# Kernel tuning notes

Measured on AMD Instinct MI355X. Metric: run time of the kernel, lower is better.

Reference implementation:

```python
import jax, jax.numpy as jnp
import numpy as np

T = 25
H1, H2, H3 = 16, 72, 32


def _lin_params(key, out_dim, in_dim):
    k1, k2 = jax.random.split(key)
    s = 1.0 / np.sqrt(in_dim)
    W = jax.random.uniform(k1, (out_dim, in_dim), jnp.float32, -s, s)
    b = jax.random.uniform(k2, (out_dim,), jnp.float32, -s, s)
    return W, b


def _lstm_params(key, in_dim, hid):
    k1, k2, k3, k4 = jax.random.split(key, 4)
    s = 1.0 / np.sqrt(hid)
    Wih = jax.random.uniform(k1, (4 * hid, in_dim), jnp.float32, -s, s)
    Whh = jax.random.uniform(k2, (4 * hid, hid), jnp.float32, -s, s)
    bih = jax.random.uniform(k3, (4 * hid,), jnp.float32, -s, s)
    bhh = jax.random.uniform(k4, (4 * hid,), jnp.float32, -s, s)
    return Wih, Whh, bih, bhh


def setup_inputs() -> dict:
    key = jax.random.key(0)
    ks = jax.random.split(key, 9)
    B = 131072
    x = jax.random.normal(ks[0], (B, T, 2), jnp.float32)
    y = jax.random.normal(ks[1], (B, T, 36), jnp.float32)
    Wih1, Whh1, bih1, bhh1 = _lstm_params(ks[2], 2, H1)
    Wih2, Whh2, bih2, bhh2 = _lstm_params(ks[3], H2, H2)
    Wih3, Whh3, bih3, bhh3 = _lstm_params(ks[4], H1 + H2, H3)
    W1, b1 = _lin_params(ks[5], 64, 36)
    W2, b2 = _lin_params(ks[6], H2, 64)
    W3, b3 = _lin_params(ks[7], 16, H3)
    W4, b4 = _lin_params(ks[8], 2, 16)
    return dict(x=x, y=y,
                Wih1=Wih1, Whh1=Whh1, bih1=bih1, bhh1=bhh1,
                Wih2=Wih2, Whh2=Whh2, bih2=bih2, bhh2=bhh2,
                Wih3=Wih3, Whh3=Whh3, bih3=bih3, bhh3=bhh3,
                W1=W1, b1=b1, W2=W2, b2=b2, W3=W3, b3=b3, W4=W4, b4=b4)


def _lstm_cell(xt, h, c, Wih, Whh, bih, bhh):
    # PyTorch LSTMCell gate order: i, f, g, o
    g = xt @ Wih.T + bih + h @ Whh.T + bhh
    i, f, gg, o = jnp.split(g, 4, axis=-1)
    c_new = jax.nn.sigmoid(f) * c + jax.nn.sigmoid(i) * jnp.tanh(gg)
    h_new = jax.nn.sigmoid(o) * jnp.tanh(c_new)
    return h_new, c_new


def _forward(x, y, Wih1, Whh1, bih1, bhh1, Wih2, Whh2, bih2, bhh2,
             Wih3, Whh3, bih3, bhh3, W1, b1, W2, b2, W3, b3, W4, b4):
    B = x.shape[0]
    init = (jnp.zeros((B, H1), jnp.float32), jnp.zeros((B, H1), jnp.float32),
            jnp.zeros((B, H2), jnp.float32), jnp.zeros((B, H2), jnp.float32),
            jnp.zeros((B, H3), jnp.float32), jnp.zeros((B, H3), jnp.float32))

    def step(carry, inp):
        h1, c1, h2, c2, h3, c3 = carry
        xt, yt = inp  # [B,2], [B,36]
        h1, c1 = _lstm_cell(xt, h1, c1, Wih1, Whh1, bih1, bhh1)
        l2 = jax.nn.relu(yt @ W1.T + b1) @ W2.T + b2
        h2, c2 = _lstm_cell(l2, h2, c2, Wih2, Whh2, bih2, bhh2)
        h = jnp.concatenate([h1, h2], axis=1)
        h3, c3 = _lstm_cell(h, h3, c3, Wih3, Whh3, bih3, bhh3)
        out = jax.nn.relu(h3 @ W3.T + b3) @ W4.T + b4  # [B,2]
        return (h1, c1, h2, c2, h3, c3), out

    xs = (jnp.swapaxes(x, 0, 1), jnp.swapaxes(y, 0, 1))  # [T,B,*]
    _, outs = jax.lax.scan(step, init, xs)  # [T,B,2]
    # torch.cat(outputs, dim=1) -> [B, T*2]
    return jnp.swapaxes(outs, 0, 1).reshape(B, T * 2)


def reference(x, y, Wih1, Whh1, bih1, bhh1, Wih2, Whh2, bih2, bhh2,
              Wih3, Whh3, bih3, bhh3, W1, b1, W2, b2, W3, b3, W4, b4):
    return _forward(x, y, Wih1, Whh1, bih1, bhh1, Wih2, Whh2, bih2, bhh2,
                    Wih3, Whh3, bih3, bhh3, W1, b1, W2, b2, W3, b3, W4, b4)
```

## Files before the change

kernel.cpp:

```cpp
#include <hip/hip_runtime.h>
#include <hip/hip_bf16.h>

#define THREADS 768

typedef __hip_bfloat16 bf16;
typedef __attribute__((ext_vector_type(4))) float f32x4;
typedef __attribute__((ext_vector_type(8))) short bf16x8;

#define MFMA __builtin_amdgcn_mfma_f32_16x16x32_bf16

#define O_A1  0
#define O_AY  4096
#define O_AT1 12288
#define O_A2  20480
#define O_AH3 40960
#define LDS_ELEMS 45056
#define LDS_BYTES (LDS_ELEMS * 2)

__device__ __forceinline__ int kmap(int l, int j) {
    return (((l >> 4) & 3) << 2) + (j & 3) + ((j >> 2) << 4);
}
__device__ __forceinline__ int frag_off(int m, int k) {
    int l = (m & 15) | (((k >> 2) & 3) << 4);
    int j = (k & 3) | (((k >> 4) & 1) << 2);
    return (l << 3) + j;
}
__device__ __forceinline__ void st_frag(bf16* sbase, int KC, int m, int k, float v) {
    sbase[(((m >> 4) * KC + (k >> 5)) << 9) + frag_off(m, k & 31)] = __float2bfloat16(v);
}
__device__ __forceinline__ void st_frag_c(bf16* sbase, int KC, int m, int cidx, int kl, float v) {
    sbase[(((m >> 4) * KC + cidx) << 9) + frag_off(m, kl)] = __float2bfloat16(v);
}

__device__ __forceinline__ float rcp_(float x) { return __builtin_amdgcn_rcpf(x); }

__device__ __forceinline__ float lstm_ew1(f32x4 acc, float& cst) {
    float ei = __expf(-acc[0]);
    float ef = __expf(-acc[1]);
    float eg = __expf(2.0f * fminf(acc[2], 40.0f));
    float eo = __expf(-acc[3]);
    float c = rcp_(1.0f + ef) * cst + (eg - 1.0f) * rcp_((1.0f + ei) * (eg + 1.0f));
    cst = c;
    float ec = __expf(2.0f * fminf(c, 40.0f));
    return (ec - 1.0f) * rcp_((1.0f + eo) * (ec + 1.0f));
}

__device__ __forceinline__ ushort bfu(float f) {
    union { bf16 b; ushort u; } v; v.b = __float2bfloat16(f); return v.u;
}

template <typename F>
__device__ __forceinline__ bf16x8 mk_frag(int lane, F val) {
    union { bf16x8 v; bf16 h[8]; } u;
#pragma unroll
    for (int j = 0; j < 8; ++j) u.h[j] = __float2bfloat16(val(kmap(lane, j)));
    return u.v;
}

__global__ void __launch_bounds__(THREADS, 3)
lstm_fused(const float* __restrict__ x, const float* __restrict__ y,
           const float* __restrict__ Wih1, const float* __restrict__ Whh1,
           const float* __restrict__ bih1, const float* __restrict__ bhh1,
           const float* __restrict__ Wih2, const float* __restrict__ Whh2,
           const float* __restrict__ bih2, const float* __restrict__ bhh2,
           const float* __restrict__ Wih3, const float* __restrict__ Whh3,
           const float* __restrict__ bih3, const float* __restrict__ bhh3,
           const float* __restrict__ W1, const float* __restrict__ b1,
           const float* __restrict__ W2, const float* __restrict__ b2,
           const float* __restrict__ W3, const float* __restrict__ b3,
           const float* __restrict__ W4, const float* __restrict__ b4,
           float* __restrict__ out) {
    extern __shared__ char smem[];
    bf16* sb = (bf16*)smem;
    const int tid = threadIdx.x;
    const int wave = tid >> 6, lane = tid & 63, ln15 = lane & 15;
    const int b0 = blockIdx.x * 64;

    const bool HEAVY = wave < 6;
    const int ntL2a = HEAVY ? 2 * wave : 6 + wave;

    bf16x8 bL2[2][5];
    bf16x8 bL1 = {};
    bf16x8 bF1[2] = {};
    bf16x8 bF2[2] = {};
    bf16x8 bL3[5] = {};
    bf16x8 bF3 = {};

    {
        auto fillL2 = [&](int nt, bf16x8* dst) {
            int R = (nt << 4) + ln15;
            int r = (R & 3) * 72 + (R >> 2);
            float bias = bih2[r] + bhh2[r];
#pragma unroll
            for (int kc = 0; kc < 5; ++kc)
                dst[kc] = mk_frag(lane, [&](int kl) {
                    int k = kc * 32 + kl;
                    return k < 72 ? Wih2[r * 72 + k]
                         : (k < 144 ? Whh2[r * 72 + (k - 72)]
                         : (k == 144 ? bias : 0.0f)); });
        };
        fillL2(ntL2a, bL2[0]);
        if (HEAVY) fillL2(2 * wave + 1, bL2[1]);
        else { bL2[1][0] = bL2[0][0]; bL2[1][1] = bL2[0][0]; bL2[1][2] = bL2[0][0];
               bL2[1][3] = bL2[0][0]; bL2[1][4] = bL2[0][0]; }
    }
    if (wave >= 6 && wave < 10) {
        int R = ((wave - 6) << 4) + ln15;
        int r = (R & 3) * 16 + (R >> 2);
        float bias = bih1[r] + bhh1[r];
        bL1 = mk_frag(lane, [&](int k) {
            return k < 2 ? Wih1[r * 2 + k]
                 : (k < 18 ? Whh1[r * 16 + (k - 2)]
                 : (k == 18 ? bias : 0.0f)); });
    }
    if (wave >= 8) {
        int n = ((wave - 8) << 4) + ln15;
        float bias = b1[n];
#pragma unroll
        for (int kc = 0; kc < 2; ++kc)
            bF1[kc] = mk_frag(lane, [&](int kl) {
                int k = kc * 32 + kl;
                return k < 36 ? W1[n * 36 + k] : (k == 36 ? bias : 0.0f); });
    }
    if (wave >= 4) {
        int R = ((wave - 4) << 4) + ln15;
        int r = (R & 3) * 32 + (R >> 2);
        float bias = bih3[r] + bhh3[r];
        bL3[0] = mk_frag(lane, [&](int k) {
            return (k >= 2 && k < 18) ? Wih3[r * 88 + (k - 2)] : (k == 18 ? bias : 0.0f); });
        bL3[1] = mk_frag(lane, [&](int k) {
            return (k >= 8) ? Wih3[r * 88 + 8 + k] : 0.0f; });
        bL3[2] = mk_frag(lane, [&](int k) { return Wih3[r * 88 + 40 + k]; });
        bL3[3] = mk_frag(lane, [&](int k) {
            return (k < 16) ? Wih3[r * 88 + 72 + k] : 0.0f; });
        bL3[4] = mk_frag(lane, [&](int k) { return Whh3[r * 32 + k]; });
    }
    if (wave < 4 || wave == 7) {
        int nt2 = (wave == 7) ? 4 : wave;
        int n = (nt2 << 4) + ln15;
#pragma unroll
        for (int kc = 0; kc < 2; ++kc)
            bF2[kc] = mk_frag(lane, [&](int kl) {
                return (n < 72) ? W2[n * 64 + kc * 32 + kl] : 0.0f; });
    }
    if (wave < 4) bF3 = mk_frag(lane, [&](int k) { return W3[ln15 * 32 + k]; });

    {
        int4* z = (int4*)sb;
        int4 zv = {0, 0, 0, 0};
        for (int i = tid; i < LDS_BYTES / 16; i += THREADS) z[i] = zv;
    }
    __syncthreads();
    for (int it = tid; it < 2 * 2304; it += THREADS) {
        int slot = it / 2304, r2 = it - slot * 2304;
        int m = r2 / 36, k = r2 - m * 36;
        st_frag(sb + O_AY + ((slot * 8) << 9), 2, m, k,
                y[(size_t)(b0 + m) * 900 + slot * 36 + k]);
    }
    if (tid < 128) {
        int m = tid >> 1, k = tid & 1;
        st_frag(sb + O_A1, 1, m, k, x[(size_t)(b0 + m) * 50 + k]);
    }
    {
        const bf16 one = __float2bfloat16(1.0f);
        if (tid < 128) {
            int s = tid >> 6, mt = (tid >> 4) & 3, n = tid & 15;
            sb[O_A1 + ((s * 4 + mt) << 9) + frag_off(n, 18)] = one;
        } else if (tid < 256) {
            int i = tid - 128; int s = i >> 6, mt = (i >> 4) & 3, n = i & 15;
            sb[O_AY + ((s * 8 + mt * 2 + 1) << 9) + frag_off(n, 4)] = one;
        } else if (tid < 384) {
            int i = tid - 256; int s = i >> 6, mt = (i >> 4) & 3, n = i & 15;
            sb[O_A2 + ((mt * 10 + 8 + s) << 9) + frag_off(n, 16)] = one;
        }
    }
    __syncthreads();
    if (wave >= 8) {
        const int nf0 = ((wave - 8) << 4) + ((lane >> 4) << 2);
#pragma unroll
        for (int s = 0; s < 2; ++s) {
#pragma unroll
            for (int mt = 0; mt < 4; ++mt) {
                f32x4 acc = {0.f, 0.f, 0.f, 0.f};
#pragma unroll
                for (int kc = 0; kc < 2; ++kc) {
                    bf16x8 a = *(const bf16x8*)(sb + O_AY + ((s * 8 + mt * 2 + kc) << 9) + (lane << 3));
                    acc = MFMA(bF1[kc], a, acc, 0, 0, 0);
                }
                int batch = (mt << 4) + ln15;
#pragma unroll
                for (int r = 0; r < 4; ++r)
                    st_frag(sb + O_AT1 + (((s ^ 1) * 8) << 9), 2, batch, nf0 + r, fmaxf(acc[r], 0.0f));
            }
        }
    }
    __syncthreads();
    if (wave < 4 || wave == 7) {
        const int nt2 = (wave == 7) ? 4 : wave;
        const int nb = (nt2 << 4) + ((lane >> 4) << 2);
        float4 bv = {0.f, 0.f, 0.f, 0.f};
        if (nb < 72) bv = *(const float4*)(b2 + nb);
#pragma unroll
        for (int mt = 0; mt < 4; ++mt) {
            f32x4 acc = {0.f, 0.f, 0.f, 0.f};
#pragma unroll
            for (int kc = 0; kc < 2; ++kc) {
                bf16x8 a = *(const bf16x8*)(sb + O_AT1 + ((8 + mt * 2 + kc) << 9) + (lane << 3));
                acc = MFMA(bF2[kc], a, acc, 0, 0, 0);
            }
            if (nb < 72) {
                int batch = (mt << 4) + ln15;
#pragma unroll
                for (int r = 0; r < 4; ++r) {
                    int n = nb + r;
                    st_frag_c(sb + O_A2, 10, batch, ((n >> 5) << 1), n & 31, acc[r] + bv[r]);
                }
            }
        }
    } else if (wave >= 10) {
        const int m = ((wave - 10) << 5) + (lane >> 1);
        const int mt = m >> 4;
        const float* yp = y + (size_t)(b0 + m) * 900 + 2 * 36;
#pragma unroll
        for (int c = (lane & 1); c < 9; c += 2) {
            float4 v = *(const float4*)(yp + 4 * c);
            ushort4 pk;
            pk.x = bfu(v.x); pk.y = bfu(v.y); pk.z = bfu(v.z); pk.w = bfu(v.w);
            int k0 = 4 * c, kc = k0 >> 5;
            int l2v = (m & 15) | (((k0 >> 2) & 3) << 4);
            int j0 = ((k0 >> 4) & 1) << 2;
            *(ushort4*)((ushort*)(sb + O_AY) + ((mt * 2 + kc) << 9) + (l2v << 3) + j0) = pk;
        }
    }
    float c1[4] = {};
    float cs2[2][4] = {};
    float c3[4] = {};
    __syncthreads();

    for (int t = 0; t <= 25; ++t) {
        const int p = t & 1, q = p ^ 1;

        if (t <= 24) {
#pragma unroll
            for (int mt = 0; mt < 4; ++mt) {
                bf16x8 al[5];
#pragma unroll
                for (int b = 0; b < 5; ++b)
                    al[b] = *(const bf16x8*)(sb + O_A2 + ((mt * 10 + 2 * b + p) << 9) + (lane << 3));
                {
                    f32x4 acc = {0.f, 0.f, 0.f, 0.f};
#pragma unroll
                    for (int b = 0; b < 5; ++b) acc = MFMA(bL2[0][b], al[b], acc, 0, 0, 0);
                    float hv = lstm_ew1(acc, cs2[0][mt]);
                    int batch = (mt << 4) + ln15;
                    int k = 72 + (ntL2a << 2) + (lane >> 4);
                    st_frag_c(sb + O_A2, 10, batch, ((k >> 5) << 1) + q, k & 31, hv);
                }
                if (HEAVY) {
                    f32x4 acc = {0.f, 0.f, 0.f, 0.f};
#pragma unroll
                    for (int b = 0; b < 5; ++b) acc = MFMA(bL2[1][b], al[b], acc, 0, 0, 0);
                    float hv = lstm_ew1(acc, cs2[1][mt]);
                    int batch = (mt << 4) + ln15;
                    int k = 72 + ((2 * wave + 1) << 2) + (lane >> 4);
                    st_frag_c(sb + O_A2, 10, batch, ((k >> 5) << 1) + q, k & 31, hv);
                }
            }
        }

        if (t <= 24 && wave >= 6 && wave < 10) {
            const int nt1 = wave - 6;
#pragma unroll
            for (int mt = 0; mt < 4; ++mt) {
                bf16x8 a = *(const bf16x8*)(sb + O_A1 + ((p * 4 + mt) << 9) + (lane << 3));
                f32x4 acc = {0.f, 0.f, 0.f, 0.f};
                acc = MFMA(bL1, a, acc, 0, 0, 0);
                float hv = lstm_ew1(acc, c1[mt]);
                int batch = (mt << 4) + ln15;
                st_frag(sb + O_A1 + ((q * 4) << 9), 1, batch, 2 + (nt1 << 2) + (lane >> 4), hv);
            }
        }
        if (wave == 6 && t <= 23) {
            const int m = lane, mt = m >> 4;
            float2 xv = *(const float2*)(x + (size_t)(b0 + m) * 50 + (t + 1) * 2);
            union { uint u; ushort s[2]; } xu;
            xu.s[0] = bfu(xv.x); xu.s[1] = bfu(xv.y);
            *(uint*)((ushort*)(sb + O_A1) + ((q * 4 + mt) << 9) + ((m & 15) << 3)) = xu.u;
        }
        if (t <= 22 && wave >= 8) {
            const int nf0 = ((wave - 8) << 4) + ((lane >> 4) << 2);
#pragma unroll
            for (int mt = 0; mt < 4; ++mt) {
                f32x4 acc = {0.f, 0.f, 0.f, 0.f};
#pragma unroll
                for (int kc = 0; kc < 2; ++kc) {
                    bf16x8 a = *(const bf16x8*)(sb + O_AY + ((p * 8 + mt * 2 + kc) << 9) + (lane << 3));
                    acc = MFMA(bF1[kc], a, acc, 0, 0, 0);
                }
                int batch = (mt << 4) + ln15;
#pragma unroll
                for (int r = 0; r < 4; ++r)
                    st_frag(sb + O_AT1 + ((q * 8) << 9), 2, batch, nf0 + r, fmaxf(acc[r], 0.0f));
            }
        }
        if (wave >= 10 && t <= 21) {
            const int m = ((wave - 10) << 5) + (lane >> 1);
            const int mt = m >> 4;
            const float* yp = y + (size_t)(b0 + m) * 900 + (t + 3) * 36;
#pragma unroll
            for (int c = (lane & 1); c < 9; c += 2) {
                float4 v = *(const float4*)(yp + 4 * c);
                ushort4 pk;
                pk.x = bfu(v.x); pk.y = bfu(v.y); pk.z = bfu(v.z); pk.w = bfu(v.w);
                int k0 = 4 * c, kc = k0 >> 5;
                int l2v = (m & 15) | (((k0 >> 2) & 3) << 4);
                int j0 = ((k0 >> 4) & 1) << 2;
                *(ushort4*)((ushort*)(sb + O_AY) + ((q * 8 + mt * 2 + kc) << 9) + (l2v << 3) + j0) = pk;
            }
        }
        if (t >= 1 && wave >= 4) {
            const int nt3 = wave - 4;
#pragma unroll
            for (int mt = 0; mt < 4; ++mt) {
                f32x4 acc = {0.f, 0.f, 0.f, 0.f};
                bf16x8 a0 = *(const bf16x8*)(sb + O_A1 + ((p * 4 + mt) << 9) + (lane << 3));
                acc = MFMA(bL3[0], a0, acc, 0, 0, 0);
#pragma unroll
                for (int j = 0; j < 3; ++j) {
                    bf16x8 a = *(const bf16x8*)(sb + O_A2 + ((mt * 10 + 4 + 2 * j + p) << 9) + (lane << 3));
                    acc = MFMA(bL3[1 + j], a, acc, 0, 0, 0);
                }
                bf16x8 a4 = *(const bf16x8*)(sb + O_AH3 + ((p * 4 + mt) << 9) + (lane << 3));
                acc = MFMA(bL3[4], a4, acc, 0, 0, 0);
                float hv = lstm_ew1(acc, c3[mt]);
                int batch = (mt << 4) + ln15;
                st_frag(sb + O_AH3 + ((q * 4) << 9), 1, batch, (nt3 << 2) + (lane >> 4), hv);
            }
        }
        if (t <= 23 && (wave < 4 || wave == 7)) {
            const int nt2 = (wave == 7) ? 4 : wave;
            const int nb = (nt2 << 4) + ((lane >> 4) << 2);
            float4 bv = {0.f, 0.f, 0.f, 0.f};
            if (nb < 72) bv = *(const float4*)(b2 + nb);
#pragma unroll
            for (int mt = 0; mt < 4; ++mt) {
                f32x4 acc = {0.f, 0.f, 0.f, 0.f};
#pragma unroll
                for (int kc = 0; kc < 2; ++kc) {
                    bf16x8 a = *(const bf16x8*)(sb + O_AT1 + ((p * 8 + mt * 2 + kc) << 9) + (lane << 3));
                    acc = MFMA(bF2[kc], a, acc, 0, 0, 0);
                }
                if (nb < 72) {
                    int batch = (mt << 4) + ln15;
#pragma unroll
                    for (int r = 0; r < 4; ++r) {
                        int n = nb + r;
                        st_frag_c(sb + O_A2, 10, batch, ((n >> 5) << 1) + q, n & 31, acc[r] + bv[r]);
                    }
                }
            }
        }
        if (t >= 2 && wave < 4) {
            const int mt = wave, qd = lane >> 4;
            float4 b3v = *(const float4*)(b3 + 4 * qd);
            float4 w0v = *(const float4*)(W4 + 4 * qd);
            float4 w1v = *(const float4*)(W4 + 16 + 4 * qd);
            bf16x8 bb = *(const bf16x8*)(sb + O_AH3 + ((p * 4 + mt) << 9) + (lane << 3));
            f32x4 acc = {0.f, 0.f, 0.f, 0.f};
            acc = MFMA(bF3, bb, acc, 0, 0, 0);
            float s0 = 0.f, s1 = 0.f;
#pragma unroll
            for (int r = 0; r < 4; ++r) {
                float u = fmaxf(acc[r] + b3v[r], 0.0f);
                s0 = fmaf(u, w0v[r], s0);
                s1 = fmaf(u, w1v[r], s1);
            }
            s0 += __shfl_xor(s0, 16); s0 += __shfl_xor(s0, 32);
            s1 += __shfl_xor(s1, 16); s1 += __shfl_xor(s1, 32);
            if (lane < 16) {
                float2 o; o.x = s0 + b4[0]; o.y = s1 + b4[1];
                *(float2*)(out + (size_t)(b0 + (mt << 4) + lane) * 50 + (t - 2) * 2) = o;
            }
        }
        __syncthreads();
    }

    if (wave < 4) {
        const int mt = wave, qd = lane >> 4;
        float4 b3v = *(const float4*)(b3 + 4 * qd);
        float4 w0v = *(const float4*)(W4 + 4 * qd);
        float4 w1v = *(const float4*)(W4 + 16 + 4 * qd);
        bf16x8 bb = *(const bf16x8*)(sb + O_AH3 + (mt << 9) + (lane << 3));
        f32x4 acc = {0.f, 0.f, 0.f, 0.f};
        acc = MFMA(bF3, bb, acc, 0, 0, 0);
        float s0 = 0.f, s1 = 0.f;
#pragma unroll
        for (int r = 0; r < 4; ++r) {
            float u = fmaxf(acc[r] + b3v[r], 0.0f);
            s0 = fmaf(u, w0v[r], s0);
            s1 = fmaf(u, w1v[r], s1);
        }
        s0 += __shfl_xor(s0, 16); s0 += __shfl_xor(s0, 32);
        s1 += __shfl_xor(s1, 16); s1 += __shfl_xor(s1, 32);
        if (lane < 16) {
            float2 o; o.x = s0 + b4[0]; o.y = s1 + b4[1];
            *(float2*)(out + (size_t)(b0 + (mt << 4) + lane) * 50 + 24 * 2) = o;
        }
    }
}

extern "C" void kernel_launch(void* const* d_in, const int* in_sizes, int n_in,
                              void* d_out, int out_size, void* d_ws, size_t ws_size,
                              hipStream_t stream) {
    (void)in_sizes; (void)n_in; (void)d_ws; (void)ws_size; (void)out_size;
    hipFuncSetAttribute((const void*)lstm_fused,
                        hipFuncAttributeMaxDynamicSharedMemorySize, LDS_BYTES);
    lstm_fused<<<dim3(2048), dim3(THREADS), LDS_BYTES, stream>>>(
        (const float*)d_in[0], (const float*)d_in[1],
        (const float*)d_in[2], (const float*)d_in[3],
        (const float*)d_in[4], (const float*)d_in[5],
        (const float*)d_in[6], (const float*)d_in[7],
        (const float*)d_in[8], (const float*)d_in[9],
        (const float*)d_in[10], (const float*)d_in[11],
        (const float*)d_in[12], (const float*)d_in[13],
        (const float*)d_in[14], (const float*)d_in[15],
        (const float*)d_in[16], (const float*)d_in[17],
        (const float*)d_in[18], (const float*)d_in[19],
        (const float*)d_in[20], (const float*)d_in[21],
        (float*)d_out);
}
```

Measured before the change: 1.001 ms.

## Switch to 32x32x16 MFMA with 16-wave role partitioning per block

Replaces the 16x16x32 bf16 MFMA tiles with 32x32x16 tiles, which changes the LDS fragment layout to a 32-column block scheme. The block grows from 12 to 16 waves, and the work is reassigned: waves 0-8 run LSTM2, waves 9-12 run LSTM3, the output head and the y prefetch, and waves 13-15 run LSTM1, the first linear layer and the second linear layer. Launch bounds go to 4 blocks of 1024 threads. The goal is fewer MFMA instructions and better balance across waves in the recurrent loop, at the cost of higher register pressure and a tighter occupancy target.

```diff
diff --git a/kernel.cpp b/kernel.cpp
--- a/kernel.cpp
+++ b/kernel.cpp
@@ -1,35 +1,29 @@
 #include <hip/hip_runtime.h>
 #include <hip/hip_bf16.h>
 
-#define THREADS 768
+#define THREADS 1024
 
 typedef __hip_bfloat16 bf16;
 typedef __attribute__((ext_vector_type(4))) float f32x4;
+typedef __attribute__((ext_vector_type(16))) float f32x16;
 typedef __attribute__((ext_vector_type(8))) short bf16x8;
 
-#define MFMA __builtin_amdgcn_mfma_f32_16x16x32_bf16
+#define MFMA32 __builtin_amdgcn_mfma_f32_32x32x16_bf16
+#define Z16 f32x16{0.f,0.f,0.f,0.f,0.f,0.f,0.f,0.f,0.f,0.f,0.f,0.f,0.f,0.f,0.f,0.f}
 
 #define O_A1  0
 #define O_AY  4096
-#define O_AT1 12288
+#define O_AT1 10240
 #define O_A2  20480
 #define O_AH3 40960
 #define LDS_ELEMS 45056
 #define LDS_BYTES (LDS_ELEMS * 2)
 
-__device__ __forceinline__ int kmap(int l, int j) {
-    return (((l >> 4) & 3) << 2) + (j & 3) + ((j >> 2) << 4);
-}
-__device__ __forceinline__ int frag_off(int m, int k) {
-    int l = (m & 15) | (((k >> 2) & 3) << 4);
-    int j = (k & 3) | (((k >> 4) & 1) << 2);
-    return (l << 3) + j;
-}
-__device__ __forceinline__ void st_frag(bf16* sbase, int KC, int m, int k, float v) {
-    sbase[(((m >> 4) * KC + (k >> 5)) << 9) + frag_off(m, k & 31)] = __float2bfloat16(v);
-}
-__device__ __forceinline__ void st_frag_c(bf16* sbase, int KC, int m, int cidx, int kl, float v) {
-    sbase[(((m >> 4) * KC + cidx) << 9) + frag_off(m, kl)] = __float2bfloat16(v);
+__device__ __forceinline__ int blk(int KC, int nt, int kc, int slot) {
+    return ((nt * KC + kc) * 2 + slot) << 9;
+}
+__device__ __forceinline__ int eix(int col, int kl) {
+    return ((col | ((kl >> 3) << 5)) << 3) + (kl & 7);
 }
 
 __device__ __forceinline__ float rcp_(float x) { return __builtin_amdgcn_rcpf(x); }
@@ -50,14 +44,15 @@
 }
 
 template <typename F>
-__device__ __forceinline__ bf16x8 mk_frag(int lane, F val) {
+__device__ __forceinline__ bf16x8 mk32(int lane, F val) {
     union { bf16x8 v; bf16 h[8]; } u;
 #pragma unroll
-    for (int j = 0; j < 8; ++j) u.h[j] = __float2bfloat16(val(kmap(lane, j)));
+    for (int j = 0; j < 8; ++j)
+        u.h[j] = __float2bfloat16(val(((lane >> 5) << 3) + j));
     return u.v;
 }
 
-__global__ void __launch_bounds__(THREADS, 3)
+__global__ void __launch_bounds__(THREADS, 4)
 lstm_fused(const float* __restrict__ x, const float* __restrict__ y,
            const float* __restrict__ Wih1, const float* __restrict__ Whh1,
            const float* __restrict__ bih1, const float* __restrict__ bhh1,
@@ -73,77 +68,77 @@
     extern __shared__ char smem[];
     bf16* sb = (bf16*)smem;
     const int tid = threadIdx.x;
-    const int wave = tid >> 6, lane = tid & 63, ln15 = lane & 15;
+    const int wave = tid >> 6, lane = tid & 63;
+    const int ln31 = lane & 31, hi = lane >> 5;
     const int b0 = blockIdx.x * 64;
 
-    const bool HEAVY = wave < 6;
-    const int ntL2a = HEAVY ? 2 * wave : 6 + wave;
-
-    bf16x8 bL2[2][5];
-    bf16x8 bL1 = {};
-    bf16x8 bF1[2] = {};
-    bf16x8 bF2[2] = {};
-    bf16x8 bL3[5] = {};
-    bf16x8 bF3 = {};
-
-    {
-        auto fillL2 = [&](int nt, bf16x8* dst) {
-            int R = (nt << 4) + ln15;
-            int r = (R & 3) * 72 + (R >> 2);
-            float bias = bih2[r] + bhh2[r];
+    bf16x8 W[11];
+#pragma unroll
+    for (int i = 0; i < 11; ++i) W[i] = bf16x8{0, 0, 0, 0, 0, 0, 0, 0};
+
+    if (wave < 9) {
+        int n = 32 * wave + ln31;
+        int r = (n & 3) * 72 + (n >> 2);
+        float bias = bih2[r] + bhh2[r];
+#pragma unroll
+        for (int kc = 0; kc < 10; ++kc)
+            W[kc] = mk32(lane, [&](int k) {
+                int kg = kc * 16 + k;
+                return kg < 72 ? Wih2[r * 72 + kg]
+                     : (kg < 144 ? Whh2[r * 72 + (kg - 72)]
+                     : (kg == 144 ? bias : 0.0f)); });
+    } else if (wave < 13) {
+        int n = 32 * (wave - 9) + ln31;
+        int r = (n & 3) * 32 + (n >> 2);
+        float bias = bih3[r] + bhh3[r];
+        W[0] = mk32(lane, [&](int k) {
+            return k < 2 ? 0.0f : Wih3[r * 88 + (k - 2)]; });
+        W[1] = mk32(lane, [&](int k) {
+            int kg = 16 + k;
+            return kg < 18 ? Wih3[r * 88 + (kg - 2)] : (kg == 18 ? bias : 0.0f); });
+#pragma unroll
+        for (int i = 0; i < 5; ++i)
+            W[2 + i] = mk32(lane, [&](int k) {
+                int kg = 64 + i * 16 + k;
+                return kg < 72 ? 0.0f : Wih3[r * 88 + 16 + (kg - 72)]; });
+#pragma unroll
+        for (int i = 0; i < 2; ++i)
+            W[7 + i] = mk32(lane, [&](int k) { return Whh3[r * 32 + i * 16 + k]; });
+        if (wave < 11) {
+#pragma unroll
+            for (int i = 0; i < 2; ++i)
+                W[9 + i] = mk32(lane, [&](int k) {
+                    return (ln31 < 16) ? W3[ln31 * 32 + i * 16 + k] : 0.0f; });
+        }
+    } else {
+        if (wave < 15) {
+            int n = 32 * (wave - 13) + ln31;
+            int r = (n & 3) * 16 + (n >> 2);
+            float bias = bih1[r] + bhh1[r];
+            W[0] = mk32(lane, [&](int k) {
+                return k < 2 ? Wih1[r * 2 + k] : Whh1[r * 16 + (k - 2)]; });
+            W[1] = mk32(lane, [&](int k) {
+                int kg = 16 + k;
+                return kg < 18 ? Whh1[r * 16 + (kg - 2)] : (kg == 18 ? bias : 0.0f); });
+        }
+        {
+            int n2 = 32 * (wave - 13) + ln31;
 #pragma unroll
             for (int kc = 0; kc < 5; ++kc)
-                dst[kc] = mk_frag(lane, [&](int kl) {
-                    int k = kc * 32 + kl;
-                    return k < 72 ? Wih2[r * 72 + k]
-                         : (k < 144 ? Whh2[r * 72 + (k - 72)]
-                         : (k == 144 ? bias : 0.0f)); });
-        };
-        fillL2(ntL2a, bL2[0]);
-        if (HEAVY) fillL2(2 * wave + 1, bL2[1]);
-        else { bL2[1][0] = bL2[0][0]; bL2[1][1] = bL2[0][0]; bL2[1][2] = bL2[0][0];
-               bL2[1][3] = bL2[0][0]; bL2[1][4] = bL2[0][0]; }
-    }
-    if (wave >= 6 && wave < 10) {
-        int R = ((wave - 6) << 4) + ln15;
-        int r = (R & 3) * 16 + (R >> 2);
-        float bias = bih1[r] + bhh1[r];
-        bL1 = mk_frag(lane, [&](int k) {
-            return k < 2 ? Wih1[r * 2 + k]
-                 : (k < 18 ? Whh1[r * 16 + (k - 2)]
-                 : (k == 18 ? bias : 0.0f)); });
-    }
-    if (wave >= 8) {
-        int n = ((wave - 8) << 4) + ln15;
-        float bias = b1[n];
-#pragma unroll
-        for (int kc = 0; kc < 2; ++kc)
-            bF1[kc] = mk_frag(lane, [&](int kl) {
-                int k = kc * 32 + kl;
-                return k < 36 ? W1[n * 36 + k] : (k == 36 ? bias : 0.0f); });
-    }
-    if (wave >= 4) {
-        int R = ((wave - 4) << 4) + ln15;
-        int r = (R & 3) * 32 + (R >> 2);
-        float bias = bih3[r] + bhh3[r];
-        bL3[0] = mk_frag(lane, [&](int k) {
-            return (k >= 2 && k < 18) ? Wih3[r * 88 + (k - 2)] : (k == 18 ? bias : 0.0f); });
-        bL3[1] = mk_frag(lane, [&](int k) {
-            return (k >= 8) ? Wih3[r * 88 + 8 + k] : 0.0f; });
-        bL3[2] = mk_frag(lane, [&](int k) { return Wih3[r * 88 + 40 + k]; });
-        bL3[3] = mk_frag(lane, [&](int k) {
-            return (k < 16) ? Wih3[r * 88 + 72 + k] : 0.0f; });
-        bL3[4] = mk_frag(lane, [&](int k) { return Whh3[r * 32 + k]; });
-    }
-    if (wave < 4 || wave == 7) {
-        int nt2 = (wave == 7) ? 4 : wave;
-        int n = (nt2 << 4) + ln15;
-#pragma unroll
-        for (int kc = 0; kc < 2; ++kc)
-            bF2[kc] = mk_frag(lane, [&](int kl) {
-                return (n < 72) ? W2[n * 64 + kc * 32 + kl] : 0.0f; });
-    }
-    if (wave < 4) bF3 = mk_frag(lane, [&](int k) { return W3[ln15 * 32 + k]; });
+                W[2 + kc] = mk32(lane, [&](int k) {
+                    int kg = kc * 16 + k;
+                    if (n2 >= 72) return 0.0f;
+                    return kg < 64 ? W2[n2 * 64 + kg] : (kg == 64 ? b2[n2] : 0.0f); });
+        }
+        if (wave >= 14) {
+            int f = 32 * (wave - 14) + ln31;
+#pragma unroll
+            for (int kc = 0; kc < 3; ++kc)
+                W[7 + kc] = mk32(lane, [&](int k) {
+                    int kg = kc * 16 + k;
+                    return kg < 36 ? W1[f * 36 + kg] : (kg == 36 ? b1[f] : 0.0f); });
+        }
+    }
 
     {
         int4* z = (int4*)sb;
@@ -154,257 +149,278 @@
     for (int it = tid; it < 2 * 2304; it += THREADS) {
         int slot = it / 2304, r2 = it - slot * 2304;
         int m = r2 / 36, k = r2 - m * 36;
-        st_frag(sb + O_AY + ((slot * 8) << 9), 2, m, k,
-                y[(size_t)(b0 + m) * 900 + slot * 36 + k]);
+        sb[O_AY + blk(3, m >> 5, k >> 4, slot) + eix(m & 31, k & 15)] =
+            __float2bfloat16(y[(size_t)(b0 + m) * 900 + slot * 36 + k]);
     }
     if (tid < 128) {
         int m = tid >> 1, k = tid & 1;
-        st_frag(sb + O_A1, 1, m, k, x[(size_t)(b0 + m) * 50 + k]);
+        sb[O_A1 + blk(2, m >> 5, 0, 0) + eix(m & 31, k)] =
+            __float2bfloat16(x[(size_t)(b0 + m) * 50 + k]);
     }
     {
         const bf16 one = __float2bfloat16(1.0f);
-        if (tid < 128) {
-            int s = tid >> 6, mt = (tid >> 4) & 3, n = tid & 15;
-            sb[O_A1 + ((s * 4 + mt) << 9) + frag_off(n, 18)] = one;
-        } else if (tid < 256) {
-            int i = tid - 128; int s = i >> 6, mt = (i >> 4) & 3, n = i & 15;
-            sb[O_AY + ((s * 8 + mt * 2 + 1) << 9) + frag_off(n, 4)] = one;
-        } else if (tid < 384) {
-            int i = tid - 256; int s = i >> 6, mt = (i >> 4) & 3, n = i & 15;
-            sb[O_A2 + ((mt * 10 + 8 + s) << 9) + frag_off(n, 16)] = one;
-        }
+        int i = tid & 127, col = i & 31, nt = (i >> 5) & 1, s = (i >> 6) & 1;
+        if (tid < 128)       sb[O_A1 + blk(2, nt, 1, s) + eix(col, 2)] = one;
+        else if (tid < 256)  sb[O_AY + blk(3, nt, 2, s) + eix(col, 4)] = one;
+        else if (tid < 384)  sb[O_AT1 + blk(5, nt, 4, s) + eix(col, 0)] = one;
+        else if (tid < 512)  sb[O_A2 + blk(10, nt, 9, s) + eix(col, 0)] = one;
     }
     __syncthreads();
-    if (wave >= 8) {
-        const int nf0 = ((wave - 8) << 4) + ((lane >> 4) << 2);
+    if (wave >= 14) {
 #pragma unroll
         for (int s = 0; s < 2; ++s) {
 #pragma unroll
-            for (int mt = 0; mt < 4; ++mt) {
-                f32x4 acc = {0.f, 0.f, 0.f, 0.f};
-#pragma unroll
-                for (int kc = 0; kc < 2; ++kc) {
-                    bf16x8 a = *(const bf16x8*)(sb + O_AY + ((s * 8 + mt * 2 + kc) << 9) + (lane << 3));
-                    acc = MFMA(bF1[kc], a, acc, 0, 0, 0);
-                }
-                int batch = (mt << 4) + ln15;
-#pragma unroll
-                for (int r = 0; r < 4; ++r)
-                    st_frag(sb + O_AT1 + (((s ^ 1) * 8) << 9), 2, batch, nf0 + r, fmaxf(acc[r], 0.0f));
+            for (int nt = 0; nt < 2; ++nt) {
+                f32x16 acc = Z16;
+#pragma unroll
+                for (int kc = 0; kc < 3; ++kc) {
+                    bf16x8 a = *(const bf16x8*)(sb + O_AY + blk(3, nt, kc, s) + (lane << 3));
+                    acc = MFMA32(W[7 + kc], a, acc, 0, 0, 0);
+                }
+#pragma unroll
+                for (int qq = 0; qq < 4; ++qq) {
+                    int f0 = 32 * (wave - 14) + 8 * qq + 4 * hi;
+                    ushort4 pk;
+                    pk.x = bfu(fmaxf(acc[4 * qq + 0], 0.f));
+                    pk.y = bfu(fmaxf(acc[4 * qq + 1], 0.f));
+                    pk.z = bfu(fmaxf(acc[4 * qq + 2], 0.f));
+                    pk.w = bfu(fmaxf(acc[4 * qq + 3], 0.f));
+                    *(ushort4*)(sb + O_AT1 + blk(5, nt, f0 >> 4, s ^ 1) + eix(ln31, f0 & 15)) = pk;
+                }
             }
         }
     }
     __syncthreads();
-    if (wave < 4 || wave == 7) {
-        const int nt2 = (wave == 7) ? 4 : wave;
-        const int nb = (nt2 << 4) + ((lane >> 4) << 2);
-        float4 bv = {0.f, 0.f, 0.f, 0.f};
-        if (nb < 72) bv = *(const float4*)(b2 + nb);
-#pragma unroll
-        for (int mt = 0; mt < 4; ++mt) {
-            f32x4 acc = {0.f, 0.f, 0.f, 0.f};
-#pragma unroll
-            for (int kc = 0; kc < 2; ++kc) {
-                bf16x8 a = *(const bf16x8*)(sb + O_AT1 + ((8 + mt * 2 + kc) << 9) + (lane << 3));
-                acc = MFMA(bF2[kc], a, acc, 0, 0, 0);
-            }
-            if (nb < 72) {
-                int batch = (mt << 4) + ln15;
-#pragma unroll
-                for (int r = 0; r < 4; ++r) {
-                    int n = nb + r;
-                    st_frag_c(sb + O_A2, 10, batch, ((n >> 5) << 1), n & 31, acc[r] + bv[r]);
-                }
-            }
-        }
-    } else if (wave >= 10) {
-        const int m = ((wave - 10) << 5) + (lane >> 1);
-        const int mt = m >> 4;
+    if (wave >= 13) {
+#pragma unroll
+        for (int nt = 0; nt < 2; ++nt) {
+            f32x16 acc = Z16;
+#pragma unroll
+            for (int kc = 0; kc < 5; ++kc) {
+                bf16x8 a = *(const bf16x8*)(sb + O_AT1 + blk(5, nt, kc, 1) + (lane << 3));
+                acc = MFMA32(W[2 + kc], a, acc, 0, 0, 0);
+            }
+#pragma unroll
+            for (int qq = 0; qq < 4; ++qq) {
+                int n0 = 32 * (wave - 13) + 8 * qq + 4 * hi;
+                if (n0 < 72) {
+                    ushort4 pk;
+                    pk.x = bfu(acc[4 * qq + 0]); pk.y = bfu(acc[4 * qq + 1]);
+                    pk.z = bfu(acc[4 * qq + 2]); pk.w = bfu(acc[4 * qq + 3]);
+                    *(ushort4*)(sb + O_A2 + blk(10, nt, n0 >> 4, 0) + eix(ln31, n0 & 15)) = pk;
+                }
+            }
+        }
+    } else if (wave == 11 || wave == 12) {
+        const int half = wave - 11;
+        const int m = 32 * half + (lane >> 1);
         const float* yp = y + (size_t)(b0 + m) * 900 + 2 * 36;
 #pragma unroll
         for (int c = (lane & 1); c < 9; c += 2) {
             float4 v = *(const float4*)(yp + 4 * c);
             ushort4 pk;
             pk.x = bfu(v.x); pk.y = bfu(v.y); pk.z = bfu(v.z); pk.w = bfu(v.w);
-            int k0 = 4 * c, kc = k0 >> 5;
-            int l2v = (m & 15) | (((k0 >> 2) & 3) << 4);
-            int j0 = ((k0 >> 4) & 1) << 2;
-            *(ushort4*)((ushort*)(sb + O_AY) + ((mt * 2 + kc) << 9) + (l2v << 3) + j0) = pk;
-        }
-    }
-    float c1[4] = {};
-    float cs2[2][4] = {};
-    float c3[4] = {};
+            int k0 = 4 * c;
+            *(ushort4*)(sb + O_AY + blk(3, half, k0 >> 4, 0) + eix(m & 31, k0 & 15)) = pk;
+        }
+    }
+    float cS[2][4] = {};
     __syncthreads();
 
     for (int t = 0; t <= 25; ++t) {
         const int p = t & 1, q = p ^ 1;
 
-        if (t <= 24) {
-#pragma unroll
-            for (int mt = 0; mt < 4; ++mt) {
-                bf16x8 al[5];
-#pragma unroll
-                for (int b = 0; b < 5; ++b)
-                    al[b] = *(const bf16x8*)(sb + O_A2 + ((mt * 10 + 2 * b + p) << 9) + (lane << 3));
-                {
-                    f32x4 acc = {0.f, 0.f, 0.f, 0.f};
-#pragma unroll
-                    for (int b = 0; b < 5; ++b) acc = MFMA(bL2[0][b], al[b], acc, 0, 0, 0);
-                    float hv = lstm_ew1(acc, cs2[0][mt]);
-                    int batch = (mt << 4) + ln15;
-                    int k = 72 + (ntL2a << 2) + (lane >> 4);
-                    st_frag_c(sb + O_A2, 10, batch, ((k >> 5) << 1) + q, k & 31, hv);
-                }
-                if (HEAVY) {
-                    f32x4 acc = {0.f, 0.f, 0.f, 0.f};
-#pragma unroll
-                    for (int b = 0; b < 5; ++b) acc = MFMA(bL2[1][b], al[b], acc, 0, 0, 0);
-                    float hv = lstm_ew1(acc, cs2[1][mt]);
-                    int batch = (mt << 4) + ln15;
-                    int k = 72 + ((2 * wave + 1) << 2) + (lane >> 4);
-                    st_frag_c(sb + O_A2, 10, batch, ((k >> 5) << 1) + q, k & 31, hv);
-                }
-            }
-        }
-
-        if (t <= 24 && wave >= 6 && wave < 10) {
-            const int nt1 = wave - 6;
-#pragma unroll
-            for (int mt = 0; mt < 4; ++mt) {
-                bf16x8 a = *(const bf16x8*)(sb + O_A1 + ((p * 4 + mt) << 9) + (lane << 3));
-                f32x4 acc = {0.f, 0.f, 0.f, 0.f};
-                acc = MFMA(bL1, a, acc, 0, 0, 0);
-                float hv = lstm_ew1(acc, c1[mt]);
-                int batch = (mt << 4) + ln15;
-                st_frag(sb + O_A1 + ((q * 4) << 9), 1, batch, 2 + (nt1 << 2) + (lane >> 4), hv);
-            }
-        }
-        if (wave == 6 && t <= 23) {
-            const int m = lane, mt = m >> 4;
-            float2 xv = *(const float2*)(x + (size_t)(b0 + m) * 50 + (t + 1) * 2);
-            union { uint u; ushort s[2]; } xu;
-            xu.s[0] = bfu(xv.x); xu.s[1] = bfu(xv.y);
-            *(uint*)((ushort*)(sb + O_A1) + ((q * 4 + mt) << 9) + ((m & 15) << 3)) = xu.u;
-        }
-        if (t <= 22 && wave >= 8) {
-            const int nf0 = ((wave - 8) << 4) + ((lane >> 4) << 2);
-#pragma unroll
-            for (int mt = 0; mt < 4; ++mt) {
-                f32x4 acc = {0.f, 0.f, 0.f, 0.f};
-#pragma unroll
-                for (int kc = 0; kc < 2; ++kc) {
-                    bf16x8 a = *(const bf16x8*)(sb + O_AY + ((p * 8 + mt * 2 + kc) << 9) + (lane << 3));
-                    acc = MFMA(bF1[kc], a, acc, 0, 0, 0);
-                }
-                int batch = (mt << 4) + ln15;
-#pragma unroll
-                for (int r = 0; r < 4; ++r)
-                    st_frag(sb + O_AT1 + ((q * 8) << 9), 2, batch, nf0 + r, fmaxf(acc[r], 0.0f));
-            }
-        }
-        if (wave >= 10 && t <= 21) {
-            const int m = ((wave - 10) << 5) + (lane >> 1);
-            const int mt = m >> 4;
-            const float* yp = y + (size_t)(b0 + m) * 900 + (t + 3) * 36;
-#pragma unroll
-            for (int c = (lane & 1); c < 9; c += 2) {
-                float4 v = *(const float4*)(yp + 4 * c);
-                ushort4 pk;
-                pk.x = bfu(v.x); pk.y = bfu(v.y); pk.z = bfu(v.z); pk.w = bfu(v.w);
-                int k0 = 4 * c, kc = k0 >> 5;
-                int l2v = (m & 15) | (((k0 >> 2) & 3) << 4);
-                int j0 = ((k0 >> 4) & 1) << 2;
-                *(ushort4*)((ushort*)(sb + O_AY) + ((q * 8 + mt * 2 + kc) << 9) + (l2v << 3) + j0) = pk;
-            }
-        }
-        if (t >= 1 && wave >= 4) {
-            const int nt3 = wave - 4;
-#pragma unroll
-            for (int mt = 0; mt < 4; ++mt) {
-                f32x4 acc = {0.f, 0.f, 0.f, 0.f};
-                bf16x8 a0 = *(const bf16x8*)(sb + O_A1 + ((p * 4 + mt) << 9) + (lane << 3));
-                acc = MFMA(bL3[0], a0, acc, 0, 0, 0);
-#pragma unroll
-                for (int j = 0; j < 3; ++j) {
-                    bf16x8 a = *(const bf16x8*)(sb + O_A2 + ((mt * 10 + 4 + 2 * j + p) << 9) + (lane << 3));
-                    acc = MFMA(bL3[1 + j], a, acc, 0, 0, 0);
-                }
-                bf16x8 a4 = *(const bf16x8*)(sb + O_AH3 + ((p * 4 + mt) << 9) + (lane << 3));
-                acc = MFMA(bL3[4], a4, acc, 0, 0, 0);
-                float hv = lstm_ew1(acc, c3[mt]);
-                int batch = (mt << 4) + ln15;
-                st_frag(sb + O_AH3 + ((q * 4) << 9), 1, batch, (nt3 << 2) + (lane >> 4), hv);
-            }
-        }
-        if (t <= 23 && (wave < 4 || wave == 7)) {
-            const int nt2 = (wave == 7) ? 4 : wave;
-            const int nb = (nt2 << 4) + ((lane >> 4) << 2);
-            float4 bv = {0.f, 0.f, 0.f, 0.f};
-            if (nb < 72) bv = *(const float4*)(b2 + nb);
-#pragma unroll
-            for (int mt = 0; mt < 4; ++mt) {
-                f32x4 acc = {0.f, 0.f, 0.f, 0.f};
-#pragma unroll
-                for (int kc = 0; kc < 2; ++kc) {
-                    bf16x8 a = *(const bf16x8*)(sb + O_AT1 + ((p * 8 + mt * 2 + kc) << 9) + (lane << 3));
-                    acc = MFMA(bF2[kc], a, acc, 0, 0, 0);
-                }
-                if (nb < 72) {
-                    int batch = (mt << 4) + ln15;
-#pragma unroll
-                    for (int r = 0; r < 4; ++r) {
-                        int n = nb + r;
-                        st_frag_c(sb + O_A2, 10, batch, ((n >> 5) << 1) + q, n & 31, acc[r] + bv[r]);
-                    }
-                }
-            }
-        }
-        if (t >= 2 && wave < 4) {
-            const int mt = wave, qd = lane >> 4;
-            float4 b3v = *(const float4*)(b3 + 4 * qd);
-            float4 w0v = *(const float4*)(W4 + 4 * qd);
-            float4 w1v = *(const float4*)(W4 + 16 + 4 * qd);
-            bf16x8 bb = *(const bf16x8*)(sb + O_AH3 + ((p * 4 + mt) << 9) + (lane << 3));
-            f32x4 acc = {0.f, 0.f, 0.f, 0.f};
-            acc = MFMA(bF3, bb, acc, 0, 0, 0);
-            float s0 = 0.f, s1 = 0.f;
-#pragma unroll
-            for (int r = 0; r < 4; ++r) {
-                float u = fmaxf(acc[r] + b3v[r], 0.0f);
-                s0 = fmaf(u, w0v[r], s0);
-                s1 = fmaf(u, w1v[r], s1);
-            }
-            s0 += __shfl_xor(s0, 16); s0 += __shfl_xor(s0, 32);
-            s1 += __shfl_xor(s1, 16); s1 += __shfl_xor(s1, 32);
-            if (lane < 16) {
-                float2 o; o.x = s0 + b4[0]; o.y = s1 + b4[1];
-                *(float2*)(out + (size_t)(b0 + (mt << 4) + lane) * 50 + (t - 2) * 2) = o;
+        if (wave < 9) {
+            if (t <= 24) {
+#pragma unroll
+                for (int nt = 0; nt < 2; ++nt) {
+                    f32x16 acc = Z16;
+#pragma unroll
+                    for (int kc = 0; kc < 10; ++kc) {
+                        bf16x8 a = *(const bf16x8*)(sb + O_A2 + blk(10, nt, kc, p) + (lane << 3));
+                        acc = MFMA32(W[kc], a, acc, 0, 0, 0);
+                    }
+#pragma unroll
+                    for (int qq = 0; qq < 4; ++qq) {
+                        f32x4 g4 = {acc[4 * qq], acc[4 * qq + 1], acc[4 * qq + 2], acc[4 * qq + 3]};
+                        float hv = lstm_ew1(g4, cS[nt][qq]);
+                        int k = 72 + 8 * wave + 2 * qq + hi;
+                        sb[O_A2 + blk(10, nt, k >> 4, q) + eix(ln31, k & 15)] = __float2bfloat16(hv);
+                    }
+                }
+            }
+        } else if (wave < 13) {
+            if (t >= 1) {
+                const int M3 = wave - 9;
+#pragma unroll
+                for (int nt = 0; nt < 2; ++nt) {
+                    f32x16 acc = Z16;
+                    {
+                        bf16x8 a0 = *(const bf16x8*)(sb + O_A1 + blk(2, nt, 0, p) + (lane << 3));
+                        acc = MFMA32(W[0], a0, acc, 0, 0, 0);
+                        bf16x8 a1 = *(const bf16x8*)(sb + O_A1 + blk(2, nt, 1, p) + (lane << 3));
+                        acc = MFMA32(W[1], a1, acc, 0, 0, 0);
+                    }
+#pragma unroll
+                    for (int i = 0; i < 5; ++i) {
+                        bf16x8 a = *(const bf16x8*)(sb + O_A2 + blk(10, nt, 4 + i, p) + (lane << 3));
+                        acc = MFMA32(W[2 + i], a, acc, 0, 0, 0);
+                    }
+#pragma unroll
+                    for (int i = 0; i < 2; ++i) {
+                        bf16x8 a = *(const bf16x8*)(sb + O_AH3 + blk(2, nt, i, p) + (lane << 3));
+                        acc = MFMA32(W[7 + i], a, acc, 0, 0, 0);
+                    }
+#pragma unroll
+                    for (int qq = 0; qq < 4; ++qq) {
+                        f32x4 g4 = {acc[4 * qq], acc[4 * qq + 1], acc[4 * qq + 2], acc[4 * qq + 3]};
+                        float hv = lstm_ew1(g4, cS[nt][qq]);
+                        int k = 8 * M3 + 2 * qq + hi;
+                        sb[O_AH3 + blk(2, nt, k >> 4, q) + eix(ln31, k & 15)] = __float2bfloat16(hv);
+                    }
+                }
+            }
+            if (wave < 11) {
+                if (t >= 2) {
+                    const int ntw = wave - 9;
+                    f32x16 acc = Z16;
+#pragma unroll
+                    for (int i = 0; i < 2; ++i) {
+                        bf16x8 a = *(const bf16x8*)(sb + O_AH3 + blk(2, ntw, i, p) + (lane << 3));
+                        acc = MFMA32(W[9 + i], a, acc, 0, 0, 0);
+                    }
+                    float s0 = 0.f, s1 = 0.f;
+#pragma unroll
+                    for (int qq = 0; qq < 2; ++qq) {
+                        int r = 8 * qq + 4 * hi;
+                        float4 b3v = *(const float4*)(b3 + r);
+                        float4 w0v = *(const float4*)(W4 + r);
+                        float4 w1v = *(const float4*)(W4 + 16 + r);
+#pragma unroll
+                        for (int s = 0; s < 4; ++s) {
+                            float u = fmaxf(acc[4 * qq + s] + b3v[s], 0.f);
+                            s0 = fmaf(u, w0v[s], s0);
+                            s1 = fmaf(u, w1v[s], s1);
+                        }
+                    }
+                    s0 += __shfl_xor(s0, 32); s1 += __shfl_xor(s1, 32);
+                    if (lane < 32) {
+                        float2 o; o.x = s0 + b4[0]; o.y = s1 + b4[1];
+                        *(float2*)(out + (size_t)(b0 + 32 * ntw + ln31) * 50 + (t - 2) * 2) = o;
+                    }
+                }
+            } else if (t <= 21) {
+                const int half = wave - 11;
+                const int m = 32 * half + (lane >> 1);
+                const float* yp = y + (size_t)(b0 + m) * 900 + (t + 3) * 36;
+#pragma unroll
+                for (int c = (lane & 1); c < 9; c += 2) {
+                    float4 v = *(const float4*)(yp + 4 * c);
+                    ushort4 pk;
+                    pk.x = bfu(v.x); pk.y = bfu(v.y); pk.z = bfu(v.z); pk.w = bfu(v.w);
+                    int k0 = 4 * c;
+                    *(ushort4*)(sb + O_AY + blk(3, half, k0 >> 4, q) + eix(m & 31, k0 & 15)) = pk;
+                }
+            }
+        } else {
+            if (t <= 24 && wave < 15) {
+                const int M1 = wave - 13;
+#pragma unroll
+                for (int nt = 0; nt < 2; ++nt) {
+                    f32x16 acc = Z16;
+#pragma unroll
+                    for (int i = 0; i < 2; ++i) {
+                        bf16x8 a = *(const bf16x8*)(sb + O_A1 + blk(2, nt, i, p) + (lane << 3));
+                        acc = MFMA32(W[i], a, acc, 0, 0, 0);
+                    }
+#pragma unroll
+                    for (int qq = 0; qq < 4; ++qq) {
+                        f32x4 g4 = {acc[4 * qq], acc[4 * qq + 1], acc[4 * qq + 2], acc[4 * qq + 3]};
+                        float hv = lstm_ew1(g4, cS[nt][qq]);
+                        int k = 2 + 8 * M1 + 2 * qq + hi;
+                        sb[O_A1 + blk(2, nt, k >> 4, q) + eix(ln31, k & 15)] = __float2bfloat16(hv);
+                    }
+                }
+            }
+            if (t <= 23 && wave == 13) {
+                const int nt = lane >> 5;
+                float2 xv = *(const float2*)(x + (size_t)(b0 + lane) * 50 + (t + 1) * 2);
+                union { uint u; ushort s[2]; } xu;
+                xu.s[0] = bfu(xv.x); xu.s[1] = bfu(xv.y);
+                *(uint*)(sb + O_A1 + blk(2, nt, 0, q) + (ln31 << 3)) = xu.u;
+            }
+            if (t <= 22 && wave >= 14) {
+#pragma unroll
+                for (int nt = 0; nt < 2; ++nt) {
+                    f32x16 acc = Z16;
+#pragma unroll
+                    for (int kc = 0; kc < 3; ++kc) {
+                        bf16x8 a = *(const bf16x8*)(sb + O_AY + blk(3, nt, kc, p) + (lane << 3));
+                        acc = MFMA32(W[7 + kc], a, acc, 0, 0, 0);
+                    }
+#pragma unroll
+                    for (int qq = 0; qq < 4; ++qq) {
+                        int f0 = 32 * (wave - 14) + 8 * qq + 4 * hi;
+                        ushort4 pk;
+                        pk.x = bfu(fmaxf(acc[4 * qq + 0], 0.f));
+                        pk.y = bfu(fmaxf(acc[4 * qq + 1], 0.f));
+                        pk.z = bfu(fmaxf(acc[4 * qq + 2], 0.f));
+                        pk.w = bfu(fmaxf(acc[4 * qq + 3], 0.f));
+                        *(ushort4*)(sb + O_AT1 + blk(5, nt, f0 >> 4, q) + eix(ln31, f0 & 15)) = pk;
+                    }
+                }
+            }
+            if (t <= 23) {
+#pragma unroll
+                for (int nt = 0; nt < 2; ++nt) {
+                    f32x16 acc = Z16;
+#pragma unroll
+                    for (int kc = 0; kc < 5; ++kc) {
+                        bf16x8 a = *(const bf16x8*)(sb + O_AT1 + blk(5, nt, kc, p) + (lane << 3));
+                        acc = MFMA32(W[2 + kc], a, acc, 0, 0, 0);
+                    }
+#pragma unroll
+                    for (int qq = 0; qq < 4; ++qq) {
+                        int n0 = 32 * (wave - 13) + 8 * qq + 4 * hi;
+                        if (n0 < 72) {
+                            ushort4 pk;
+                            pk.x = bfu(acc[4 * qq + 0]); pk.y = bfu(acc[4 * qq + 1]);
+                            pk.z = bfu(acc[4 * qq + 2]); pk.w = bfu(acc[4 * qq + 3]);
+                            *(ushort4*)(sb + O_A2 + blk(10, nt, n0 >> 4, q) + eix(ln31, n0 & 15)) = pk;
+                        }
+                    }
+                }
             }
         }
         __syncthreads();
     }
 
-    if (wave < 4) {
-        const int mt = wave, qd = lane >> 4;
-        float4 b3v = *(const float4*)(b3 + 4 * qd);
-        float4 w0v = *(const float4*)(W4 + 4 * qd);
-        float4 w1v = *(const float4*)(W4 + 16 + 4 * qd);
-        bf16x8 bb = *(const bf16x8*)(sb + O_AH3 + (mt << 9) + (lane << 3));
-        f32x4 acc = {0.f, 0.f, 0.f, 0.f};
-        acc = MFMA(bF3, bb, acc, 0, 0, 0);
+    if (wave == 9 || wave == 10) {
+        const int ntw = wave - 9;
+        f32x16 acc = Z16;
+#pragma unroll
+        for (int i = 0; i < 2; ++i) {
+            bf16x8 a = *(const bf16x8*)(sb + O_AH3 + blk(2, ntw, i, 0) + (lane << 3));
+            acc = MFMA32(W[9 + i], a, acc, 0, 0, 0);
+        }
         float s0 = 0.f, s1 = 0.f;
 #pragma unroll
-        for (int r = 0; r < 4; ++r) {
-            float u = fmaxf(acc[r] + b3v[r], 0.0f);
-            s0 = fmaf(u, w0v[r], s0);
-            s1 = fmaf(u, w1v[r], s1);
-        }
-        s0 += __shfl_xor(s0, 16); s0 += __shfl_xor(s0, 32);
-        s1 += __shfl_xor(s1, 16); s1 += __shfl_xor(s1, 32);
-        if (lane < 16) {
+        for (int qq = 0; qq < 2; ++qq) {
+            int r = 8 * qq + 4 * hi;
+            float4 b3v = *(const float4*)(b3 + r);
+            float4 w0v = *(const float4*)(W4 + r);
+            float4 w1v = *(const float4*)(W4 + 16 + r);
+#pragma unroll
+            for (int s = 0; s < 4; ++s) {
+                float u = fmaxf(acc[4 * qq + s] + b3v[s], 0.f);
+                s0 = fmaf(u, w0v[s], s0);
+                s1 = fmaf(u, w1v[s], s1);
+            }
+        }
+        s0 += __shfl_xor(s0, 32); s1 += __shfl_xor(s1, 32);
+        if (lane < 32) {
             float2 o; o.x = s0 + b4[0]; o.y = s1 + b4[1];
-            *(float2*)(out + (size_t)(b0 + (mt << 4) + lane) * 50 + 24 * 2) = o;
+            *(float2*)(out + (size_t)(b0 + 32 * ntw + ln31) * 50 + 24 * 2) = o;
         }
     }
 }
```

Measured after the change: 944.3 us. 1.06x faster.
